# Kernel optimization log

Measured on AMD Instinct MI355X. Metric: run time of the kernel, lower is better.

The kernel has to match this reference:

```python
import jax, jax.numpy as jnp
import numpy as np

D = 1024
L_COMP = 16384
L_FULL = 32768
EPS = 1e-4


def setup_inputs() -> dict:
    key = jax.random.key(0)
    k1, k2 = jax.random.split(key)
    x = jax.random.normal(k1, (1, L_COMP, D), dtype=jnp.float32)
    p_selected = jax.random.uniform(k2, (L_COMP,), dtype=jnp.float32)
    # boundary mask over full sequence: exactly L_COMP ones, first position forced to 1
    rng = np.random.default_rng(0)
    pos = np.concatenate([[0], np.sort(rng.choice(np.arange(1, L_FULL), L_COMP - 1, replace=False))])
    b_np = np.zeros((1, L_FULL), dtype=np.int32)
    b_np[0, pos] = 1
    b = jnp.asarray(b_np)
    return {"x": x, "p_selected": p_selected, "b": b}


def _ema_scan(x, p):
    # z_t = (1 - p_t) * z_{t-1} + p_t * x_t  (exact math of the mamba chunk scan
    # with A=-1, dt=log(1/(1-p)), B=p, C=1, x pre-divided by dt)
    a = jnp.broadcast_to((1.0 - p)[None, :, None], x.shape)  # (1, L, d) decay
    bxt = p[None, :, None] * x                                # (1, L, d) input term

    def combine(c1, c2):
        a1, b1 = c1
        a2, b2 = c2
        return a1 * a2, a2 * b1 + b2

    _, z = jax.lax.associative_scan(combine, (a, bxt), axis=1)
    return z


def reference(x, p_selected, b):
    p = jnp.clip(p_selected.astype(jnp.float32), EPS, 1.0 - EPS)  # (L_comp,)
    z_bar = _ema_scan(x.astype(jnp.float32), p)                   # (1, L_comp, d)
    plug_back_idx = jnp.cumsum(b, axis=1) - 1                     # (1, L_full)
    out = jnp.take(z_bar[0], plug_back_idx[0], axis=0)[None]      # (1, L_full, d)
    return out.astype(x.dtype)
```

## Files before the change

kernel.cpp:

```cpp
#include <hip/hip_runtime.h>


#define DCH 1024
#define L_COMP 16384
#define L_FULL 32768
#define CHUNK 32
#define NCHUNK (L_COMP / CHUNK)
#define SEG (L_FULL / NCHUNK)
#define NTHR 512
#define EPSV 1e-4f
#define WMIN 1e-12f

typedef float v2f __attribute__((ext_vector_type(2)));

__device__ __forceinline__ float clipp(float p) {
    p = fmaxf(p, EPSV);
    return fminf(p, 1.0f - EPSV);
}

__global__ __launch_bounds__(NTHR, 4) void fused_kernel(
    const float* __restrict__ x, const float* __restrict__ p,
    const int* __restrict__ b, float* __restrict__ out) {
    const int c = blockIdx.x;
    const int tid = threadIdx.x;
    const int lane = tid & 63;
    const int wave = tid >> 6;
    const int base = c * CHUNK;

    __shared__ int bpref[NCHUNK + 1];
    __shared__ int spos[CHUNK + 1];
    __shared__ int wtot[8];

    {
        const int4* bseg = reinterpret_cast<const int4*>(b) + tid * (SEG / 4);
        int v = 0;
#pragma unroll 4
        for (int q = 0; q < SEG / 4; ++q) {
            int4 w = bseg[q];
            v += w.x + w.y + w.z + w.w;
        }
        int incl = v;
#pragma unroll
        for (int off = 1; off < 64; off <<= 1) {
            int n = __shfl_up(incl, off, 64);
            if (lane >= off) incl += n;
        }
        if (lane == 63) wtot[wave] = incl;
        __syncthreads();
        int woff = 0;
        for (int w = 0; w < wave; ++w) woff += wtot[w];
        bpref[tid] = woff + incl - v;
        if (tid == 0) bpref[NCHUNK] = L_COMP;
        __syncthreads();
    }

    if (tid <= CHUNK) {
        int t = base + tid;
        int posv = L_FULL;
        if (t < L_COMP) {
            int lo = 0, hi = NCHUNK;
            while (hi - lo > 1) {
                int mid = (lo + hi) >> 1;
                if (bpref[mid] <= t) lo = mid; else hi = mid;
            }
            int lr = t - bpref[lo];
            const int4* bseg = reinterpret_cast<const int4*>(b) + lo * (SEG / 4);
            int cnt = 0;
#pragma unroll 4
            for (int q = 0; q < SEG / 4; ++q) {
                int4 w = bseg[q];
                if (w.x) { if (cnt == lr) posv = lo * SEG + 4 * q + 0; ++cnt; }
                if (w.y) { if (cnt == lr) posv = lo * SEG + 4 * q + 1; ++cnt; }
                if (w.z) { if (cnt == lr) posv = lo * SEG + 4 * q + 2; ++cnt; }
                if (w.w) { if (cnt == lr) posv = lo * SEG + 4 * q + 3; ++cnt; }
            }
        }
        spos[tid] = posv;
    }
    __syncthreads();

    int kstart = c;
    {
        float w = 1.0f;
        while (kstart > 0 && w >= WMIN) {
            --kstart;
            float ap = 1.0f;
#pragma unroll 8
            for (int t = 0; t < CHUNK; ++t)
                ap *= (1.0f - clipp(p[kstart * CHUNK + t]));
            w *= ap;
        }
    }

    const v2f* x2 = reinterpret_cast<const v2f*>(x) + tid;
    v2f h = (v2f)0.f;
    for (int r = kstart * CHUNK; r < base; r += 8) {
        v2f xw[8];
        float pw[8];
#pragma unroll
        for (int j = 0; j < 8; ++j) {
            xw[j] = x2[(size_t)(r + j) * (DCH / 2)];
            pw[j] = clipp(p[r + j]);
        }
#pragma unroll
        for (int j = 0; j < 8; ++j) {
            float a = 1.0f - pw[j];
            h = a * h + pw[j] * xw[j];
        }
    }

    v2f xv[CHUNK];
#pragma unroll
    for (int j = 0; j < CHUNK; ++j)
        xv[j] = x2[(size_t)(base + j) * (DCH / 2)];

#pragma unroll
    for (int j = 0; j < CHUNK; ++j) {
        float pt = clipp(p[base + j]);
        float a = 1.0f - pt;
        h = a * h + pt * xv[j];
        xv[j] = h;
    }

    {
        v2f* out2 = reinterpret_cast<v2f*>(out) + tid;
        int f0 = spos[0];
#pragma unroll
        for (int j = 0; j < CHUNK; ++j) {
            int f1 = spos[j + 1];
            for (int f = f0; f < f1; ++f)
                __builtin_nontemporal_store(xv[j], &out2[(size_t)f * (DCH / 2)]);
            f0 = f1;
        }
    }
}

extern "C" void kernel_launch(void* const* d_in, const int* in_sizes, int n_in,
                              void* d_out, int out_size, void* d_ws, size_t ws_size,
                              hipStream_t stream) {
    const float* x = (const float*)d_in[0];
    const float* p = (const float*)d_in[1];
    const int* b = (const int*)d_in[2];
    float* out = (float*)d_out;
    (void)d_ws; (void)ws_size;

    fused_kernel<<<NCHUNK, NTHR, 0, stream>>>(x, p, b, out);
}
```

Baseline: 205.0 us.

## Replace per-block lookback rescan with decoupled lookback over published chunk states

```diff
diff --git a/kernel.cpp b/kernel.cpp
--- a/kernel.cpp
+++ b/kernel.cpp
@@ -20,16 +20,48 @@
 
 __global__ __launch_bounds__(NTHR, 4) void fused_kernel(
     const float* __restrict__ x, const float* __restrict__ p,
-    const int* __restrict__ b, float* __restrict__ out) {
-    const int c = blockIdx.x;
+    const int* __restrict__ b, float* __restrict__ out,
+    float* __restrict__ Bbuf, float* __restrict__ Apub,
+    int* __restrict__ flag, int* __restrict__ ticket) {
     const int tid = threadIdx.x;
     const int lane = tid & 63;
     const int wave = tid >> 6;
-    const int base = c * CHUNK;
 
     __shared__ int bpref[NCHUNK + 1];
     __shared__ int spos[CHUNK + 1];
     __shared__ int wtot[8];
+    __shared__ int vcs;
+
+    if (tid == 0) vcs = atomicAdd(ticket, 1);
+    __syncthreads();
+    const int c = vcs;
+    const int base = c * CHUNK;
+
+    const v2f* x2 = reinterpret_cast<const v2f*>(x) + tid;
+    v2f xv[CHUNK];
+#pragma unroll
+    for (int j = 0; j < CHUNK; ++j)
+        xv[j] = x2[(size_t)(base + j) * (DCH / 2)];
+
+    float aprod = 1.0f;
+    {
+        v2f h = (v2f)0.f;
+#pragma unroll
+        for (int j = 0; j < CHUNK; ++j) {
+            float pt = clipp(p[base + j]);
+            float a = 1.0f - pt;
+            h = a * h + pt * xv[j];
+            xv[j] = h;
+            aprod *= a;
+        }
+        reinterpret_cast<v2f*>(Bbuf)[c * (DCH / 2) + tid] = h;
+    }
+    if (tid == 0) Apub[c] = aprod;
+    __syncthreads();
+    if (tid == 0) {
+        __threadfence();
+        __hip_atomic_store(&flag[c], 1, __ATOMIC_RELEASE, __HIP_MEMORY_SCOPE_AGENT);
+    }
 
     {
         const int4* bseg = reinterpret_cast<const int4*>(b) + tid * (SEG / 4);
@@ -79,47 +111,30 @@
     }
     __syncthreads();
 
-    int kstart = c;
+    v2f hpre = (v2f)0.f;
     {
         float w = 1.0f;
-        while (kstart > 0 && w >= WMIN) {
-            --kstart;
-            float ap = 1.0f;
-#pragma unroll 8
-            for (int t = 0; t < CHUNK; ++t)
-                ap *= (1.0f - clipp(p[kstart * CHUNK + t]));
-            w *= ap;
+        const v2f* B2 = reinterpret_cast<const v2f*>(Bbuf) + tid;
+        for (int k = c - 1; k >= 0; --k) {
+            if (w < WMIN) break;
+            while (__hip_atomic_load(&flag[k], __ATOMIC_ACQUIRE,
+                                     __HIP_MEMORY_SCOPE_AGENT) == 0)
+                __builtin_amdgcn_s_sleep(1);
+            v2f bk = B2[(size_t)k * (DCH / 2)];
+            float ak = Apub[k];
+            hpre += w * bk;
+            w *= ak;
         }
     }
 
-    const v2f* x2 = reinterpret_cast<const v2f*>(x) + tid;
-    v2f h = (v2f)0.f;
-    for (int r = kstart * CHUNK; r < base; r += 8) {
-        v2f xw[8];
-        float pw[8];
+    {
+        float ap = 1.0f;
 #pragma unroll
-        for (int j = 0; j < 8; ++j) {
-            xw[j] = x2[(size_t)(r + j) * (DCH / 2)];
-            pw[j] = clipp(p[r + j]);
+        for (int j = 0; j < CHUNK; ++j) {
+            float pt = clipp(p[base + j]);
+            ap *= (1.0f - pt);
+            xv[j] = xv[j] + ap * hpre;
         }
-#pragma unroll
-        for (int j = 0; j < 8; ++j) {
-            float a = 1.0f - pw[j];
-            h = a * h + pw[j] * xw[j];
-        }
-    }
-
-    v2f xv[CHUNK];
-#pragma unroll
-    for (int j = 0; j < CHUNK; ++j)
-        xv[j] = x2[(size_t)(base + j) * (DCH / 2)];
-
-#pragma unroll
-    for (int j = 0; j < CHUNK; ++j) {
-        float pt = clipp(p[base + j]);
-        float a = 1.0f - pt;
-        h = a * h + pt * xv[j];
-        xv[j] = h;
     }
 
     {
@@ -142,7 +157,13 @@
     const float* p = (const float*)d_in[1];
     const int* b = (const int*)d_in[2];
     float* out = (float*)d_out;
-    (void)d_ws; (void)ws_size;
 
-    fused_kernel<<<NCHUNK, NTHR, 0, stream>>>(x, p, b, out);
+    char* ws = (char*)d_ws;
+    float* Apub = (float*)ws;
+    int* flag = (int*)(ws + 4096);
+    int* ticket = (int*)(ws + 6144);
+    float* Bbuf = (float*)(ws + 8192);
+
+    hipMemsetAsync(ws + 4096, 0, 4096, stream);
+    fused_kernel<<<NCHUNK, NTHR, 0, stream>>>(x, p, b, out, Bbuf, Apub, flag, ticket);
 }
```

Result: slower. 257.5 us (+25.6%).
